# Performance work log

Hardware: AMD Instinct MI355X
Metric: run time of the kernel (lower is better)

## Reference

```python
import jax, jax.numpy as jnp
import numpy as np

N_POINTS = 8192
N_DIM = 2
N_PAIRS = 262144


def setup_inputs() -> dict:
    key = jax.random.key(0)
    k1, k2, k3, k4 = jax.random.split(key, 4)
    logits = jax.random.normal(k1, (N_POINTS, N_DIM), dtype=jnp.float32)
    i = jax.random.randint(k2, (N_PAIRS,), 0, N_POINTS, dtype=jnp.int64)
    j = jax.random.randint(k3, (N_PAIRS,), 0, N_POINTS, dtype=jnp.int64)
    pij = jax.random.uniform(k4, (N_PAIRS,), dtype=jnp.float32, minval=1e-6, maxval=1.0)
    pij = pij / jnp.sum(pij)  # joint probabilities, strictly positive
    return {"pij": pij, "i": i, "j": j, "logits": logits}


def reference(pij, i, j, logits):
    # Pairwise squared distances via the norm expansion (same math as the
    # N x N x D expanded-subtract in the torch original, without the huge tensor).
    sq = jnp.sum(logits * logits, axis=1)                      # [N]
    dkl2 = sq[:, None] + sq[None, :] - 2.0 * (logits @ logits.T)  # [N, N]
    n_diag = logits.shape[0]
    # Student-t partition function, excluding the diagonal (each diag term is 1).
    part = jnp.sum(1.0 / (1.0 + dkl2)) - n_diag
    xi = logits[i]                                              # [E, D]
    xj = logits[j]                                              # [E, D]
    # NOTE: torch adds 1.0 elementwise BEFORE summing over D, so this is
    # (D + ||xi-xj||^2)^-1 — reproduced faithfully.
    num = 1.0 / jnp.sum(1.0 + (xi - xj) ** 2, axis=1)           # [E]
    qij = num / part
    return jnp.sum(pij * (jnp.log(pij) - jnp.log(qij)))
```

## Files before the change

### kernel.cpp

```cpp
#include <hip/hip_runtime.h>
#include <math.h>

#define N_POINTS 8192
#define N_PAIRS  262144

constexpr int BLOCKS  = 512;
constexpr int THREADS = 256;
constexpr int TILE    = 8;
constexpr int NTILES  = N_POINTS / TILE;
constexpr int EPB     = N_PAIRS / BLOCKS;

__global__ __launch_bounds__(THREADS)
void fused_kernel(const float* __restrict__ logits,
                  const float* __restrict__ pij,
                  const int* __restrict__ ei,
                  const int* __restrict__ ej,
                  float* __restrict__ partials) {
    __shared__ float2 pts[N_POINTS];
    __shared__ float wred[3][THREADS / 64];

    const int t = threadIdx.x;
    const int b = blockIdx.x;

    {
        const float4* src = (const float4*)logits;
        float4* dst = (float4*)pts;
        #pragma unroll
        for (int k = t; k < N_POINTS / 2; k += THREADS) dst[k] = src[k];
    }
    __syncthreads();

    const int v1 = b;
    const int v2 = NTILES - 1 - b;

    auto sweep = [&](int v) -> float {
        const int r0 = v * TILE;
        float rx[TILE], ry[TILE];
        #pragma unroll
        for (int r = 0; r < TILE; ++r) { rx[r] = pts[r0 + r].x; ry[r] = pts[r0 + r].y; }
        float a[TILE];
        #pragma unroll
        for (int r = 0; r < TILE; ++r) a[r] = 0.0f;
        #pragma unroll 2
        for (int k = r0 + t; k < N_POINTS; k += THREADS) {
            const float2 q = pts[k];
            #pragma unroll
            for (int r = 0; r < TILE; ++r) {
                const float dx = rx[r] - q.x;
                const float dy = ry[r] - q.y;
                const float d2 = __builtin_fmaf(dx, dx, __builtin_fmaf(dy, dy, 1.0f));
                a[r] += __builtin_amdgcn_rcpf(d2);
            }
        }
        float s = 0.0f;
        #pragma unroll
        for (int r = 0; r < TILE; ++r) s += a[r];
        return s;
    };

    float T = sweep(v1) + sweep(v2);

    float Dc = 0.0f;
    if (t < 128) {
        const int v = (t < 64) ? v1 : v2;
        const int l = t & 63;
        const int i = v * TILE + (l >> 3);
        const int k = v * TILE + (l & 7);
        const float dx = pts[i].x - pts[k].x;
        const float dy = pts[i].y - pts[k].y;
        const float d2 = __builtin_fmaf(dx, dx, __builtin_fmaf(dy, dy, 1.0f));
        Dc = __builtin_amdgcn_rcpf(d2);
    }
    float part = __builtin_fmaf(2.0f, T, -Dc);

    float s1 = 0.0f, sp = 0.0f;
    {
        const int2   ea = ((const int2*)(ei + b * EPB))[t];
        const int2   eb = ((const int2*)(ej + b * EPB))[t];
        const float2 pp = ((const float2*)(pij + b * EPB))[t];

        float2 pa = pts[ea.x], pb = pts[eb.x];
        float dx = pa.x - pb.x, dy = pa.y - pb.y;
        float d2 = __builtin_fmaf(dx, dx, __builtin_fmaf(dy, dy, 2.0f));
        s1 += pp.x * (__logf(pp.x) + __logf(d2));
        sp += pp.x;

        pa = pts[ea.y]; pb = pts[eb.y];
        dx = pa.x - pb.x; dy = pa.y - pb.y;
        d2 = __builtin_fmaf(dx, dx, __builtin_fmaf(dy, dy, 2.0f));
        s1 += pp.y * (__logf(pp.y) + __logf(d2));
        sp += pp.y;
    }

    #pragma unroll
    for (int off = 32; off > 0; off >>= 1) {
        part += __shfl_down(part, off, 64);
        s1   += __shfl_down(s1,   off, 64);
        sp   += __shfl_down(sp,   off, 64);
    }
    const int w = t >> 6, l = t & 63;
    if (l == 0) { wred[0][w] = part; wred[1][w] = s1; wred[2][w] = sp; }
    __syncthreads();
    if (t == 0) {
        float r0s = 0.f, r1s = 0.f, r2s = 0.f;
        #pragma unroll
        for (int i = 0; i < THREADS / 64; ++i) {
            r0s += wred[0][i]; r1s += wred[1][i]; r2s += wred[2][i];
        }
        partials[0 * BLOCKS + b] = r0s;
        partials[1 * BLOCKS + b] = r1s;
        partials[2 * BLOCKS + b] = r2s;
    }
}

__global__ __launch_bounds__(256)
void final_kernel(const float* __restrict__ partials, float* __restrict__ out) {
    __shared__ double ra[4], rs[4], rp[4];
    const int t = threadIdx.x;

    double a = (double)partials[0 * BLOCKS + t] + (double)partials[0 * BLOCKS + t + 256];
    double s = (double)partials[1 * BLOCKS + t] + (double)partials[1 * BLOCKS + t + 256];
    double p = (double)partials[2 * BLOCKS + t] + (double)partials[2 * BLOCKS + t + 256];

    #pragma unroll
    for (int off = 32; off > 0; off >>= 1) {
        a += __shfl_down(a, off, 64);
        s += __shfl_down(s, off, 64);
        p += __shfl_down(p, off, 64);
    }
    const int w = t >> 6, l = t & 63;
    if (l == 0) { ra[w] = a; rs[w] = s; rp[w] = p; }
    __syncthreads();
    if (t == 0) {
        double A = 0.0, S = 0.0, P = 0.0;
        #pragma unroll
        for (int i = 0; i < 4; ++i) { A += ra[i]; S += rs[i]; P += rp[i]; }
        A -= (double)N_POINTS;
        out[0] = (float)(S + log(A) * P);
    }
}

extern "C" void kernel_launch(void* const* d_in, const int* in_sizes, int n_in,
                              void* d_out, int out_size, void* d_ws, size_t ws_size,
                              hipStream_t stream) {
    const float* pij    = (const float*)d_in[0];
    const int*   ei     = (const int*)d_in[1];
    const int*   ej     = (const int*)d_in[2];
    const float* logits = (const float*)d_in[3];
    float* out = (float*)d_out;

    float* partials = (float*)d_ws;

    fused_kernel<<<BLOCKS, THREADS, 0, stream>>>(logits, pij, ei, ej, partials);
    final_kernel<<<1, 256, 0, stream>>>(partials, out);
}
```

Before: 73.03 us.

## Fuse final reduction via last-block ticket and halve block count

```diff
diff --git a/kernel.cpp b/kernel.cpp
--- a/kernel.cpp
+++ b/kernel.cpp
@@ -4,10 +4,11 @@
 #define N_POINTS 8192
 #define N_PAIRS  262144
 
-constexpr int BLOCKS  = 512;
-constexpr int THREADS = 256;
+constexpr int BLOCKS  = 256;
+constexpr int THREADS = 512;
 constexpr int TILE    = 8;
 constexpr int NTILES  = N_POINTS / TILE;
+constexpr int TPB     = 4;
 constexpr int EPB     = N_PAIRS / BLOCKS;
 
 __global__ __launch_bounds__(THREADS)
@@ -15,9 +16,13 @@
                   const float* __restrict__ pij,
                   const int* __restrict__ ei,
                   const int* __restrict__ ej,
-                  float* __restrict__ partials) {
+                  unsigned int* __restrict__ ticket,
+                  float* __restrict__ partials,
+                  float* __restrict__ out) {
     __shared__ float2 pts[N_POINTS];
     __shared__ float wred[3][THREADS / 64];
+    __shared__ double dred[3][4];
+    __shared__ int is_last;
 
     const int t = threadIdx.x;
     const int b = blockIdx.x;
@@ -30,17 +35,17 @@
     }
     __syncthreads();
 
-    const int v1 = b;
-    const int v2 = NTILES - 1 - b;
+    const int tiles[TPB] = { b, 511 - b, 512 + b, 1023 - b };
 
-    auto sweep = [&](int v) -> float {
-        const int r0 = v * TILE;
-        float rx[TILE], ry[TILE];
+    float T = 0.0f;
+    #pragma unroll
+    for (int ti = 0; ti < TPB; ++ti) {
+        const int r0 = tiles[ti] * TILE;
+        float rx[TILE], ry[TILE], a[TILE];
         #pragma unroll
-        for (int r = 0; r < TILE; ++r) { rx[r] = pts[r0 + r].x; ry[r] = pts[r0 + r].y; }
-        float a[TILE];
-        #pragma unroll
-        for (int r = 0; r < TILE; ++r) a[r] = 0.0f;
+        for (int r = 0; r < TILE; ++r) {
+            rx[r] = pts[r0 + r].x; ry[r] = pts[r0 + r].y; a[r] = 0.0f;
+        }
         #pragma unroll 2
         for (int k = r0 + t; k < N_POINTS; k += THREADS) {
             const float2 q = pts[k];
@@ -52,17 +57,13 @@
                 a[r] += __builtin_amdgcn_rcpf(d2);
             }
         }
-        float s = 0.0f;
         #pragma unroll
-        for (int r = 0; r < TILE; ++r) s += a[r];
-        return s;
-    };
-
-    float T = sweep(v1) + sweep(v2);
+        for (int r = 0; r < TILE; ++r) T += a[r];
+    }
 
     float Dc = 0.0f;
-    if (t < 128) {
-        const int v = (t < 64) ? v1 : v2;
+    if (t < 64 * TPB) {
+        const int v = tiles[t >> 6];
         const int l = t & 63;
         const int i = v * TILE + (l >> 3);
         const int k = v * TILE + (l & 7);
@@ -110,33 +111,41 @@
         partials[0 * BLOCKS + b] = r0s;
         partials[1 * BLOCKS + b] = r1s;
         partials[2 * BLOCKS + b] = r2s;
+        __threadfence();
+        const unsigned int old = __hip_atomic_fetch_add(
+            ticket, 1u, __ATOMIC_ACQ_REL, __HIP_MEMORY_SCOPE_AGENT);
+        is_last = (old == (unsigned int)(BLOCKS - 1));
     }
-}
+    __syncthreads();
 
-__global__ __launch_bounds__(256)
-void final_kernel(const float* __restrict__ partials, float* __restrict__ out) {
-    __shared__ double ra[4], rs[4], rp[4];
-    const int t = threadIdx.x;
-
-    double a = (double)partials[0 * BLOCKS + t] + (double)partials[0 * BLOCKS + t + 256];
-    double s = (double)partials[1 * BLOCKS + t] + (double)partials[1 * BLOCKS + t + 256];
-    double p = (double)partials[2 * BLOCKS + t] + (double)partials[2 * BLOCKS + t + 256];
-
-    #pragma unroll
-    for (int off = 32; off > 0; off >>= 1) {
-        a += __shfl_down(a, off, 64);
-        s += __shfl_down(s, off, 64);
-        p += __shfl_down(p, off, 64);
-    }
-    const int w = t >> 6, l = t & 63;
-    if (l == 0) { ra[w] = a; rs[w] = s; rp[w] = p; }
-    __syncthreads();
-    if (t == 0) {
-        double A = 0.0, S = 0.0, P = 0.0;
+    if (is_last) {
+        __threadfence();
+        double a = 0.0, s = 0.0, p = 0.0;
+        if (t < BLOCKS) {
+            a = (double)__hip_atomic_load(&partials[0 * BLOCKS + t],
+                                          __ATOMIC_RELAXED, __HIP_MEMORY_SCOPE_AGENT);
+            s = (double)__hip_atomic_load(&partials[1 * BLOCKS + t],
+                                          __ATOMIC_RELAXED, __HIP_MEMORY_SCOPE_AGENT);
+            p = (double)__hip_atomic_load(&partials[2 * BLOCKS + t],
+                                          __ATOMIC_RELAXED, __HIP_MEMORY_SCOPE_AGENT);
+        }
         #pragma unroll
-        for (int i = 0; i < 4; ++i) { A += ra[i]; S += rs[i]; P += rp[i]; }
-        A -= (double)N_POINTS;
-        out[0] = (float)(S + log(A) * P);
+        for (int off = 32; off > 0; off >>= 1) {
+            a += __shfl_down(a, off, 64);
+            s += __shfl_down(s, off, 64);
+            p += __shfl_down(p, off, 64);
+        }
+        if (l == 0 && t < BLOCKS) { dred[0][w] = a; dred[1][w] = s; dred[2][w] = p; }
+        __syncthreads();
+        if (t == 0) {
+            double A = 0.0, S = 0.0, P = 0.0;
+            #pragma unroll
+            for (int i = 0; i < BLOCKS / 64; ++i) {
+                A += dred[0][i]; S += dred[1][i]; P += dred[2][i];
+            }
+            A -= (double)N_POINTS;
+            out[0] = (float)(S + log(A) * P);
+        }
     }
 }
 
@@ -149,8 +158,10 @@
     const float* logits = (const float*)d_in[3];
     float* out = (float*)d_out;
 
-    float* partials = (float*)d_ws;
+    unsigned int* ticket = (unsigned int*)d_ws;
+    float* partials = (float*)((char*)d_ws + 64);
 
-    fused_kernel<<<BLOCKS, THREADS, 0, stream>>>(logits, pij, ei, ej, partials);
-    final_kernel<<<1, 256, 0, stream>>>(partials, out);
+    hipMemsetAsync(ticket, 0, sizeof(unsigned int), stream);
+    fused_kernel<<<BLOCKS, THREADS, 0, stream>>>(logits, pij, ei, ej,
+                                                 ticket, partials, out);
 }
```

Measured after the change: 80.50 us. 1.1x slower.
